# Kernel tuning notes

Measured on AMD Instinct MI355X. Metric: run time of the kernel, lower is better.

The kernel has to match this reference:

```python
import jax, jax.numpy as jnp
import numpy as np

B, N, F = 256, 64, 64
S = 2 * N + 2  # seq_len = N*2 + 2 = 130
EPS = 1e-6
SCALE = float(np.sqrt(S))


def _norm(x, alpha, beta):
    # custom Norm: mean/std over last axis, affine params shaped (F, S)
    m = jnp.mean(x, axis=-1, keepdims=True)
    s = jnp.std(x, axis=-1, keepdims=True)
    return alpha * (x - m) / (s + EPS) + beta


def setup_inputs() -> dict:
    key = jax.random.key(0)
    ks = jax.random.split(key, 12)
    d = {
        "sp": jax.random.normal(ks[0], (B, F), jnp.float32),
        "h1": jax.random.normal(ks[1], (B, N, F), jnp.float32),
        "h2": jax.random.normal(ks[2], (B, N, F), jnp.float32),
        # Dense(seq_len) kernels act on last axis of length S
        "Wq": jax.random.normal(ks[3], (S, S), jnp.float32) * 0.05,
        "bq": jnp.zeros((S,), jnp.float32),
        "Wk": jax.random.normal(ks[4], (S, S), jnp.float32) * 0.05,
        "bk": jnp.zeros((S,), jnp.float32),
        "Wv": jax.random.normal(ks[5], (S, S), jnp.float32) * 0.05,
        "bv": jnp.zeros((S,), jnp.float32),
        "alpha1": jnp.ones((F, S), jnp.float32),
        "beta1": jnp.zeros((F, S), jnp.float32),
        "alpha2": jnp.ones((F, S), jnp.float32),
        "beta2": jnp.zeros((F, S), jnp.float32),
        "Wlin": jax.random.normal(ks[6], (F * S, 1), jnp.float32) * 0.02,
        "blin": jnp.zeros((1,), jnp.float32),
    }
    return d


def reference(sp, h1, h2, Wq, bq, Wk, bk, Wv, bv,
              alpha1, beta1, alpha2, beta2, Wlin, blin):
    # obs: (B, 2N+1, F) -> transpose -> (B, F, 2N+1)
    obs = jnp.concatenate((h1, h2, sp[:, None, :]), axis=1).transpose(0, 2, 1)
    h2t = h2.transpose(0, 2, 1)  # (B, F, N): each action is a (B, F) column

    def fwd_action(action):  # action: (B, F)
        x = jnp.concatenate((obs, action[:, :, None]), axis=-1)  # (B, F, S)
        xn = _norm(x, alpha1, beta1)
        q = xn @ Wq + bq  # (B, F, S)
        k = xn @ Wk + bk
        v = xn @ Wv + bv
        # attention over the FEATURE axis: scores (B, F, F)
        sim = jnp.einsum('bis,bjs->bij', q, k) / SCALE
        p = jax.nn.softmax(sim, axis=-1)
        ao = jnp.einsum('bij,bjs->bis', p, v)  # (B, F, S)
        # deterministic dropout => residual is ao + ao
        y = _norm(ao + ao, alpha2, beta2)
        return y.reshape(B, -1) @ Wlin + blin  # (B, 1)

    q_values = jax.vmap(fwd_action, in_axes=-1, out_axes=1)(h2t)  # (B, N, 1)
    return q_values.reshape(B, N)
```

## Files before the change

kernel.cpp:

```cpp
#include <hip/hip_runtime.h>
#include <math.h>


typedef __attribute__((ext_vector_type(4))) float f32x4;
typedef __attribute__((ext_vector_type(8))) _Float16 h8;

#define EPSF 1e-6f
#define INVS 0.0877058019307029f

__device__ __forceinline__ unsigned short f2h(float f) {
  _Float16 h = (_Float16)f;
  return __builtin_bit_cast(unsigned short, h);
}
__device__ __forceinline__ float h2f(unsigned short s) {
  return (float)__builtin_bit_cast(_Float16, s);
}
__device__ __forceinline__ unsigned int pkh(float a, float b) {
  unsigned int r;
  asm("v_cvt_pkrtz_f16_f32 %0, %1, %2" : "=v"(r) : "v"(a), "v"(b));
  return r;
}

__global__ __launch_bounds__(256) void k0(
    const float* __restrict__ alpha1, const float* __restrict__ beta1,
    const float* __restrict__ alpha2, const float* __restrict__ beta2,
    const float* __restrict__ Wq, const float* __restrict__ bq,
    const float* __restrict__ Wk, const float* __restrict__ bk,
    const float* __restrict__ Wv, const float* __restrict__ bv,
    const float* __restrict__ Wlin, const float* __restrict__ blin,
    unsigned short* __restrict__ ABqk, unsigned short* __restrict__ ABv,
    unsigned short* __restrict__ AWt, float* __restrict__ Paw, float* __restrict__ Ccw)
{
  __shared__ float sbuf[64 * 132];
  __shared__ float Wbuf[130 * 144];
  int blk = blockIdx.x, tid = threadIdx.x;
  if (blk < 6) {
    int m = blk >> 1, isB = blk & 1;
    const float* src  = isB ? beta1 : alpha1;
    const float* W    = (m == 0) ? Wq : (m == 1) ? Wk : Wv;
    const float* bias = (m == 0) ? bq : (m == 1) ? bk : bv;
    for (int e = tid; e < 8320; e += 256) { int f = e / 130, s = e - f * 130; sbuf[f * 132 + s] = src[e]; }
    for (int e = tid; e < 16900; e += 256) { int s = e / 130, t = e - s * 130; Wbuf[s * 144 + t] = W[e]; }
    __syncthreads();
    int ty = tid >> 4, tx = tid & 15;
    float acc[4][9] = {};
    for (int s = 0; s < 130; ++s) {
      float g0 = sbuf[(ty * 4 + 0) * 132 + s];
      float g1 = sbuf[(ty * 4 + 1) * 132 + s];
      float g2 = sbuf[(ty * 4 + 2) * 132 + s];
      float g3 = sbuf[(ty * 4 + 3) * 132 + s];
#pragma unroll
      for (int c = 0; c < 9; ++c) {
        float wv = Wbuf[s * 144 + tx + 16 * c];
        acc[0][c] += g0 * wv; acc[1][c] += g1 * wv;
        acc[2][c] += g2 * wv; acc[3][c] += g3 * wv;
      }
    }
#pragma unroll
    for (int i = 0; i < 4; ++i)
      for (int c = 0; c < 9; ++c) {
        int t = tx + 16 * c;
        if (t < 136) {
          float val = (t < 130) ? (acc[i][c] + (isB ? bias[t] : 0.f)) : 0.f;
          unsigned short v16 = f2h(val);
          int f = ty * 4 + i;
          if (m == 2) ABv[t * 128 + isB * 64 + f] = v16;
          else        ABqk[(m * 64 + f) * 272 + (t >> 3) * 16 + isB * 8 + (t & 7)] = v16;
        }
      }
  } else if (blk == 6) {
    if (tid < 64) {
      int f = tid;
      float pa = 0.f, cc = 0.f;
      for (int s = 0; s < 130; ++s) {
        float wl = Wlin[f * 130 + s];
        float aw = alpha2[f * 130 + s] * wl;
        AWt[s * 72 + f] = f2h(aw);
        pa += aw;
        cc += beta2[f * 130 + s] * wl;
      }
      for (int s = 130; s < 144; ++s) AWt[s * 72 + f] = 0;
      Paw[f] = pa;
#pragma unroll
      for (int msk = 1; msk <= 32; msk <<= 1) cc += __shfl_xor(cc, msk, 64);
      if (f == 0) Ccw[0] = cc + blin[0];
    }
  }
}

__global__ __launch_bounds__(256) void k1(
    const float* __restrict__ h1, const float* __restrict__ h2,
    const float* __restrict__ sp, const float* __restrict__ alpha1,
    const float* __restrict__ Wq, const float* __restrict__ Wk, const float* __restrict__ Wv,
    unsigned short* __restrict__ UqkB, unsigned short* __restrict__ UvB,
    float* __restrict__ S1g, float* __restrict__ S2g)
{
  __shared__ float gbuf[64 * 132];
  __shared__ float Wbuf[130 * 144];
  __shared__ float ps[2][256];
  int b = blockIdx.x, tid = threadIdx.x;
  float s1 = 0.f, s2 = 0.f;
  for (int idx = tid; idx < 8256; idx += 256) {
    int s = idx >> 6, f = idx & 63;
    float x = (s < 64)  ? h1[((size_t)(b * 64 + s)) * 64 + f]
            : (s < 128) ? h2[((size_t)(b * 64 + (s - 64))) * 64 + f]
                        : sp[b * 64 + f];
    gbuf[f * 132 + s] = alpha1[f * 130 + s] * x;
    s1 += x; s2 += x * x;
  }
  ps[0][tid] = s1; ps[1][tid] = s2;
  __syncthreads();
  if (tid < 64) {
    S1g[b * 64 + tid] = ps[0][tid] + ps[0][tid + 64] + ps[0][tid + 128] + ps[0][tid + 192];
    S2g[b * 64 + tid] = ps[1][tid] + ps[1][tid + 64] + ps[1][tid + 128] + ps[1][tid + 192];
  }
  int ty = tid >> 4, tx = tid & 15;
  for (int m = 0; m < 3; ++m) {
    const float* W = (m == 0) ? Wq : (m == 1) ? Wk : Wv;
    __syncthreads();
    for (int e = tid; e < 16900; e += 256) { int s = e / 130, t = e - s * 130; Wbuf[s * 144 + t] = W[e]; }
    __syncthreads();
    float acc[4][9] = {};
    for (int s = 0; s < 129; ++s) {
      float g0 = gbuf[(ty * 4 + 0) * 132 + s];
      float g1 = gbuf[(ty * 4 + 1) * 132 + s];
      float g2 = gbuf[(ty * 4 + 2) * 132 + s];
      float g3 = gbuf[(ty * 4 + 3) * 132 + s];
#pragma unroll
      for (int c = 0; c < 9; ++c) {
        float wv = Wbuf[s * 144 + tx + 16 * c];
        acc[0][c] += g0 * wv; acc[1][c] += g1 * wv;
        acc[2][c] += g2 * wv; acc[3][c] += g3 * wv;
      }
    }
#pragma unroll
    for (int i = 0; i < 4; ++i)
      for (int c = 0; c < 9; ++c) {
        int t = tx + 16 * c;
        if (t < 136) {
          unsigned short v16 = f2h((t < 130) ? acc[i][c] : 0.f);
          int f = ty * 4 + i;
          if (m == 2) UvB[((size_t)b * 136 + t) * 64 + f] = v16;
          else        UqkB[(((size_t)b * 2 + m) * 64 + f) * 136 + t] = v16;
        }
      }
  }
}

__global__ __launch_bounds__(512, 2) void k2(
    const float* __restrict__ h2, const float* __restrict__ alpha1,
    const unsigned short* __restrict__ UqkB, const unsigned short* __restrict__ UvB,
    const unsigned short* __restrict__ ABqk, const unsigned short* __restrict__ ABv,
    const unsigned short* __restrict__ AWt,
    const float* __restrict__ S1g, const float* __restrict__ S2g,
    const float* __restrict__ Paw, const float* __restrict__ Ccw,
    const float* __restrict__ Wq, const float* __restrict__ Wk, const float* __restrict__ Wv,
    float* __restrict__ out)
{
  __shared__ __align__(16) unsigned short qb[64 * 168];
  __shared__ __align__(16) unsigned short kb[64 * 168];
  __shared__ __align__(16) unsigned short vT[144 * 72];
  __shared__ __align__(16) unsigned short pb[64 * 72];
  __shared__ __align__(16) unsigned short w129h[3][136];
  __shared__ float S1l[64], S2l[64], ael[64];
  __shared__ __align__(16) unsigned short mrow[64], irow[64], crow[64];
  __shared__ float redbuf[4];

  int bh = blockIdx.x;
  int b = bh >> 1, n0 = (bh & 1) << 5;
  int tid = threadIdx.x;
  int w = tid >> 6, l = tid & 63, l15 = l & 15, l4 = l >> 4;

  if (tid < 136) {
    w129h[0][tid] = (tid < 130) ? f2h(Wq[129 * 130 + tid]) : (unsigned short)0;
    w129h[1][tid] = (tid < 130) ? f2h(Wk[129 * 130 + tid]) : (unsigned short)0;
    w129h[2][tid] = (tid < 130) ? f2h(Wv[129 * 130 + tid]) : (unsigned short)0;
  }
  if (tid >= 256 && tid < 320) {
    int ff = tid - 256;
    float s1v = S1g[b * 64 + ff];
    float s2v = S2g[b * 64 + ff];
    float aev = alpha1[ff * 130 + 129];
    S1l[ff] = s1v; S2l[ff] = s2v; ael[ff] = aev;
    float a  = h2[((size_t)(b * 64 + n0)) * 64 + ff];
    float m  = (s1v + a) * (1.f / 130.f);
    float e2 = (s2v + a * a) * (1.f / 130.f);
    float sd = sqrtf(fmaxf(e2 - m * m, 0.f));
    mrow[ff] = f2h(m);
    irow[ff] = f2h(1.f / (sd + EPSF));
    crow[ff] = f2h(ael[ff] * a);
  }
  for (int i = tid; i < 64 * 24; i += 512) {
    int ff = i / 24, t = 136 + (i - ff * 24);
    qb[ff * 168 + t] = 0; kb[ff * 168 + t] = 0;
  }
  for (int i = tid; i < 14 * 72; i += 512) vT[130 * 72 + i] = 0;

  float awr[9][4], pawr[4];
  if (w < 4) {
#pragma unroll
    for (int sf = 0; sf < 9; ++sf)
#pragma unroll
      for (int rr = 0; rr < 4; ++rr)
        awr[sf][rr] = h2f(AWt[(sf * 16 + l15) * 72 + w * 16 + l4 * 4 + rr]);
#pragma unroll
    for (int rr = 0; rr < 4; ++rr) pawr[rr] = Paw[w * 16 + l4 * 4 + rr];
  }
  float ccv = Ccw[0];

  int isK = tid >> 8, t5 = tid & 255;
  const unsigned short* uqkg = UqkB + ((size_t)b * 2 + isK) * 64 * 136;
  const unsigned short* abg  = ABqk + isK * 64 * 272;
  const unsigned short* uvg  = UvB + (size_t)b * 136 * 64;
  unsigned short* dstqk = isK ? kb : qb;

  auto ldu = [&](int o) { int fo = o / 17, g = o - fo * 17;
                          return *(const h8*)(uqkg + fo * 136 + g * 8); };
  auto lda = [&](int o) { int fo = o / 17, g = o - fo * 17;
                          return *(const h8*)(abg + fo * 272 + g * 16); };
  auto ldb = [&](int o) { int fo = o / 17, g = o - fo * 17;
                          return *(const h8*)(abg + fo * 272 + g * 16 + 8); };
  h8 qU0 = ldu(t5),       qA0 = lda(t5),       qB0 = ldb(t5);
  h8 qU1 = ldu(t5 + 256), qA1 = lda(t5 + 256), qB1 = ldb(t5 + 256);
  h8 qU2 = ldu(t5 + 512), qA2 = lda(t5 + 512), qB2 = ldb(t5 + 512);
  h8 qU3 = ldu(t5 + 768), qA3 = lda(t5 + 768), qB3 = ldb(t5 + 768);
  h8 qUt = {}, qAt = {}, qBt = {};
  if (t5 < 64) { qUt = ldu(1024 + t5); qAt = lda(1024 + t5); qBt = ldb(1024 + t5); }
  auto ldvu = [&](int o) { int t = o >> 3, vf = o & 7;
                           return *(const h8*)(uvg + t * 64 + vf * 8); };
  auto ldva = [&](int o) { int t = o >> 3, vf = o & 7;
                           return *(const h8*)(ABv + t * 128 + (o & 7) * 8); };
  auto ldvb = [&](int o) { int t = o >> 3;
                           return *(const h8*)(ABv + t * 128 + 64 + (o & 7) * 8); };
  h8 vU0 = ldvu(tid),       vA0 = ldva(tid),       vB0 = ldvb(tid);
  h8 vU1 = ldvu(tid + 512), vA1 = ldva(tid + 512), vB1 = ldvb(tid + 512);
  h8 vUt = {}, vAt = {}, vBt = {};
  if (tid < 16) { vUt = ldvu(1024 + tid); vAt = ldva(1024 + tid); vBt = ldvb(1024 + tid); }

  __syncthreads();

  auto genqk = [&](int o, h8 uu, h8 aa, h8 bb) {
    int fo = o / 17, g = o - fo * 17;
    _Float16 m   = __builtin_bit_cast(_Float16, mrow[fo]);
    _Float16 inv = __builtin_bit_cast(_Float16, irow[fo]);
    _Float16 c   = __builtin_bit_cast(_Float16, crow[fo]);
    h8 ww = *(const h8*)(&w129h[isK][g * 8]);
    h8 res = (uu + c * ww - m * aa) * inv + bb;
    *(h8*)(dstqk + fo * 168 + g * 8) = res;
  };
  auto genv = [&](int o, h8 uu, h8 aa, h8 bb) {
    int t = o >> 3, vf = o & 7;
    _Float16 wv = __builtin_bit_cast(_Float16, w129h[2][t]);
    h8 mv = *(const h8*)(&mrow[vf * 8]);
    h8 iv = *(const h8*)(&irow[vf * 8]);
    h8 cv = *(const h8*)(&crow[vf * 8]);
    h8 res = (uu + cv * wv - mv * aa) * iv + bb;
    *(h8*)(&vT[t * 72 + vf * 8]) = res;
  };

  for (int n = n0; n < n0 + 32; ++n) {
    if (n > n0 && tid == 0)
      out[b * 64 + n - 1] = redbuf[0] + redbuf[1] + redbuf[2] + redbuf[3] + ccv;
    genqk(t5,       qU0, qA0, qB0);
    genqk(t5 + 256, qU1, qA1, qB1);
    genqk(t5 + 512, qU2, qA2, qB2);
    genqk(t5 + 768, qU3, qA3, qB3);
    if (t5 < 64) genqk(1024 + t5, qUt, qAt, qBt);
    genv(tid,       vU0, vA0, vB0);
    genv(tid + 512, vU1, vA1, vB1);
    if (tid < 16) genv(1024 + tid, vUt, vAt, vBt);
    __syncthreads();

    if (w < 4) {
      f32x4 sacc[4] = {};
      {
        const unsigned short* qrow = &qb[(w * 16 + l15) * 168 + l4 * 8];
#pragma unroll
        for (int kk = 0; kk < 5; ++kk) {
          h8 avv = *(const h8*)&qrow[kk * 32];
#pragma unroll
          for (int cf = 0; cf < 4; ++cf) {
            h8 bvv = *(const h8*)&kb[(cf * 16 + l15) * 168 + l4 * 8 + kk * 32];
            sacc[cf] = __builtin_amdgcn_mfma_f32_16x16x32_f16(avv, bvv, sacc[cf], 0, 0, 0);
          }
        }
      }
      float prob[4][4];
#pragma unroll
      for (int rr = 0; rr < 4; ++rr) {
        float ssum = 0.f;
#pragma unroll
        for (int cf = 0; cf < 4; ++cf) {
          float e = __expf(sacc[cf][rr] * INVS);
          prob[cf][rr] = e;
          ssum += e;
        }
#pragma unroll
        for (int msk = 1; msk <= 8; msk <<= 1) ssum += __shfl_xor(ssum, msk, 64);
        float is = 1.f / ssum;
#pragma unroll
        for (int cf = 0; cf < 4; ++cf) prob[cf][rr] *= is;
      }
#pragma unroll
      for (int cf = 0; cf < 4; ++cf) {
        unsigned int p01 = pkh(prob[cf][0], prob[cf][1]);
        unsigned int p23 = pkh(prob[cf][2], prob[cf][3]);
        int base = (w * 16 + l4 * 4) * 72 + cf * 16 + l15;
        pb[base]       = (unsigned short)p01;
        pb[base + 72]  = (unsigned short)(p01 >> 16);
        pb[base + 144] = (unsigned short)p23;
        pb[base + 216] = (unsigned short)(p23 >> 16);
      }

      f32x4 ao[9] = {};
      {
        const unsigned short* prow = &pb[(w * 16 + l15) * 72 + l4 * 8];
#pragma unroll
        for (int kk = 0; kk < 2; ++kk) {
          h8 avv = *(const h8*)&prow[kk * 32];
#pragma unroll
          for (int sf = 0; sf < 9; ++sf) {
            h8 bvv = *(const h8*)&vT[(sf * 16 + l15) * 72 + l4 * 8 + kk * 32];
            ao[sf] = __builtin_amdgcn_mfma_f32_16x16x32_f16(avv, bvv, ao[sf], 0, 0, 0);
          }
        }
      }
      float csum = 0.f;
#pragma unroll
      for (int rr = 0; rr < 4; ++rr) {
        float s1 = 0.f, s2 = 0.f, sdt = 0.f;
#pragma unroll
        for (int sf = 0; sf < 9; ++sf) {
          float v = ao[sf][rr];
          s1 += v; s2 += v * v; sdt += v * awr[sf][rr];
        }
#pragma unroll
        for (int msk = 1; msk <= 8; msk <<= 1) {
          s1 += __shfl_xor(s1, msk, 64);
          s2 += __shfl_xor(s2, msk, 64);
          sdt += __shfl_xor(sdt, msk, 64);
        }
        float mz  = 2.f * s1 * (1.f / 130.f);
        float ez2 = 4.f * s2 * (1.f / 130.f);
        float sg  = sqrtf(fmaxf(ez2 - mz * mz, 0.f));
        float i2  = 1.f / (sg + EPSF);
        csum += (2.f * sdt - mz * pawr[rr]) * i2;
      }
      csum += __shfl_xor(csum, 16, 64);
      csum += __shfl_xor(csum, 32, 64);
      if (l == 0) redbuf[w] = csum;
    } else if (w == 4 && n < n0 + 31) {
      int ff = l;
      float a  = h2[((size_t)(b * 64 + n + 1)) * 64 + ff];
      float m  = (S1l[ff] + a) * (1.f / 130.f);
      float e2 = (S2l[ff] + a * a) * (1.f / 130.f);
      float sd = sqrtf(fmaxf(e2 - m * m, 0.f));
      mrow[ff] = f2h(m);
      irow[ff] = f2h(1.f / (sd + EPSF));
      crow[ff] = f2h(ael[ff] * a);
    }
    __syncthreads();
  }
  if (tid == 0)
    out[b * 64 + n0 + 31] = redbuf[0] + redbuf[1] + redbuf[2] + redbuf[3] + ccv;
}

extern "C" void kernel_launch(void* const* d_in, const int* in_sizes, int n_in,
                              void* d_out, int out_size, void* d_ws, size_t ws_size,
                              hipStream_t stream) {
  const float* sp     = (const float*)d_in[0];
  const float* h1     = (const float*)d_in[1];
  const float* h2     = (const float*)d_in[2];
  const float* Wq     = (const float*)d_in[3];
  const float* bq     = (const float*)d_in[4];
  const float* Wk     = (const float*)d_in[5];
  const float* bk     = (const float*)d_in[6];
  const float* Wv     = (const float*)d_in[7];
  const float* bv     = (const float*)d_in[8];
  const float* alpha1 = (const float*)d_in[9];
  const float* beta1  = (const float*)d_in[10];
  const float* alpha2 = (const float*)d_in[11];
  const float* beta2  = (const float*)d_in[12];
  const float* Wlin   = (const float*)d_in[13];
  const float* blin   = (const float*)d_in[14];
  float* out = (float*)d_out;

  unsigned short* UqkB = (unsigned short*)d_ws;
  unsigned short* UvB  = UqkB + 4456448;
  unsigned short* ABqk = UvB + 2228224;
  unsigned short* ABv  = ABqk + 34816;
  unsigned short* AWt  = ABv + 17408;
  float* S1g = (float*)(AWt + 10368);
  float* S2g = S1g + 16384;
  float* Paw = S2g + 16384;
  float* Ccw = Paw + 64;

  k0<<<dim3(7), dim3(256), 0, stream>>>(alpha1, beta1, alpha2, beta2,
                                        Wq, bq, Wk, bk, Wv, bv, Wlin, blin,
                                        ABqk, ABv, AWt, Paw, Ccw);
  k1<<<dim3(256), dim3(256), 0, stream>>>(h1, h2, sp, alpha1, Wq, Wk, Wv,
                                          UqkB, UvB, S1g, S2g);
  k2<<<dim3(512), dim3(512), 0, stream>>>(h2, alpha1, UqkB, UvB, ABqk, ABv, AWt,
                                          S1g, S2g, Paw, Ccw,
                                          Wq, Wk, Wv, out);
}
```

Before: 343.5 us.

## Double-buffer q/k/v LDS tiles and process all actions per block

The q/k/v and norm-row shared buffers are double-buffered so each iteration generates the next action's tiles while computing the current one. This cuts the per-action loop from two barriers to one. Each block now handles all 64 actions of a batch row, so the grid shrinks from 512 to 256 blocks. The larger LDS footprint likely allows only one block per CU, which gives up the inter-block overlap the old two-blocks-per-CU layout provided and doubles the serial iterations per block.

```diff
diff --git a/kernel.cpp b/kernel.cpp
--- a/kernel.cpp
+++ b/kernel.cpp
@@ -157,18 +157,16 @@
     const float* __restrict__ Wq, const float* __restrict__ Wk, const float* __restrict__ Wv,
     float* __restrict__ out)
 {
-  __shared__ __align__(16) unsigned short qb[64 * 168];
-  __shared__ __align__(16) unsigned short kb[64 * 168];
-  __shared__ __align__(16) unsigned short vT[144 * 72];
+  __shared__ __align__(16) unsigned short qb[2][64 * 168];
+  __shared__ __align__(16) unsigned short kb[2][64 * 168];
+  __shared__ __align__(16) unsigned short vT[2][144 * 72];
   __shared__ __align__(16) unsigned short pb[64 * 72];
   __shared__ __align__(16) unsigned short w129h[3][136];
   __shared__ float S1l[64], S2l[64], ael[64];
-  __shared__ __align__(16) unsigned short mrow[64], irow[64], crow[64];
-  __shared__ float redbuf[4];
-
-  int bh = blockIdx.x;
-  int b = bh >> 1, n0 = (bh & 1) << 5;
-  int tid = threadIdx.x;
+  __shared__ __align__(16) unsigned short mrowB[2][64], irowB[2][64], crowB[2][64];
+  __shared__ float redbuf[2][4];
+
+  int b = blockIdx.x, tid = threadIdx.x;
   int w = tid >> 6, l = tid & 63, l15 = l & 15, l4 = l >> 4;
 
   if (tid < 136) {
@@ -176,25 +174,32 @@
     w129h[1][tid] = (tid < 130) ? f2h(Wk[129 * 130 + tid]) : (unsigned short)0;
     w129h[2][tid] = (tid < 130) ? f2h(Wv[129 * 130 + tid]) : (unsigned short)0;
   }
-  if (tid >= 256 && tid < 320) {
-    int ff = tid - 256;
-    float s1v = S1g[b * 64 + ff];
-    float s2v = S2g[b * 64 + ff];
-    float aev = alpha1[ff * 130 + 129];
-    S1l[ff] = s1v; S2l[ff] = s2v; ael[ff] = aev;
-    float a  = h2[((size_t)(b * 64 + n0)) * 64 + ff];
-    float m  = (s1v + a) * (1.f / 130.f);
-    float e2 = (s2v + a * a) * (1.f / 130.f);
+  if (tid >= 192 && tid < 256) {
+    int ff = tid - 192;
+    S1l[ff] = S1g[b * 64 + ff];
+    S2l[ff] = S2g[b * 64 + ff];
+    ael[ff] = alpha1[ff * 130 + 129];
+  }
+  if (tid < 128) {
+    int nn = tid >> 6, ff = tid & 63;
+    float a  = h2[((size_t)(b * 64 + nn)) * 64 + ff];
+    float s1 = S1g[b * 64 + ff], s2 = S2g[b * 64 + ff];
+    float m  = (s1 + a) * (1.f / 130.f);
+    float e2 = (s2 + a * a) * (1.f / 130.f);
     float sd = sqrtf(fmaxf(e2 - m * m, 0.f));
-    mrow[ff] = f2h(m);
-    irow[ff] = f2h(1.f / (sd + EPSF));
-    crow[ff] = f2h(ael[ff] * a);
-  }
-  for (int i = tid; i < 64 * 24; i += 512) {
-    int ff = i / 24, t = 136 + (i - ff * 24);
-    qb[ff * 168 + t] = 0; kb[ff * 168 + t] = 0;
-  }
-  for (int i = tid; i < 14 * 72; i += 512) vT[130 * 72 + i] = 0;
+    mrowB[nn][ff] = f2h(m);
+    irowB[nn][ff] = f2h(1.f / (sd + EPSF));
+    crowB[nn][ff] = f2h(alpha1[ff * 130 + 129] * a);
+  }
+  for (int i = tid; i < 2 * 64 * 24; i += 512) {
+    int c = i / (64 * 24), j = i - c * (64 * 24);
+    int ff = j / 24, t = 136 + (j - ff * 24);
+    qb[c][ff * 168 + t] = 0; kb[c][ff * 168 + t] = 0;
+  }
+  for (int i = tid; i < 2 * 14 * 72; i += 512) {
+    int c = i / (14 * 72), j = i - c * (14 * 72);
+    vT[c][130 * 72 + j] = 0;
+  }
 
   float awr[9][4], pawr[4];
   if (w < 4) {
@@ -212,7 +217,6 @@
   const unsigned short* uqkg = UqkB + ((size_t)b * 2 + isK) * 64 * 136;
   const unsigned short* abg  = ABqk + isK * 64 * 272;
   const unsigned short* uvg  = UvB + (size_t)b * 136 * 64;
-  unsigned short* dstqk = isK ? kb : qb;
 
   auto ldu = [&](int o) { int fo = o / 17, g = o - fo * 17;
                           return *(const h8*)(uqkg + fo * 136 + g * 8); };
@@ -229,9 +233,9 @@
   auto ldvu = [&](int o) { int t = o >> 3, vf = o & 7;
                            return *(const h8*)(uvg + t * 64 + vf * 8); };
   auto ldva = [&](int o) { int t = o >> 3, vf = o & 7;
-                           return *(const h8*)(ABv + t * 128 + (o & 7) * 8); };
-  auto ldvb = [&](int o) { int t = o >> 3;
-                           return *(const h8*)(ABv + t * 128 + 64 + (o & 7) * 8); };
+                           return *(const h8*)(ABv + t * 128 + vf * 8); };
+  auto ldvb = [&](int o) { int t = o >> 3, vf = o & 7;
+                           return *(const h8*)(ABv + t * 128 + 64 + vf * 8); };
   h8 vU0 = ldvu(tid),       vA0 = ldva(tid),       vB0 = ldvb(tid);
   h8 vU1 = ldvu(tid + 512), vA1 = ldva(tid + 512), vB1 = ldvb(tid + 512);
   h8 vUt = {}, vAt = {}, vBt = {};
@@ -239,48 +243,59 @@
 
   __syncthreads();
 
-  auto genqk = [&](int o, h8 uu, h8 aa, h8 bb) {
+  auto genqk = [&](int o, h8 uu, h8 aa, h8 bb, int sl, unsigned short* dstb) {
     int fo = o / 17, g = o - fo * 17;
-    _Float16 m   = __builtin_bit_cast(_Float16, mrow[fo]);
-    _Float16 inv = __builtin_bit_cast(_Float16, irow[fo]);
-    _Float16 c   = __builtin_bit_cast(_Float16, crow[fo]);
+    _Float16 m   = __builtin_bit_cast(_Float16, mrowB[sl][fo]);
+    _Float16 inv = __builtin_bit_cast(_Float16, irowB[sl][fo]);
+    _Float16 c   = __builtin_bit_cast(_Float16, crowB[sl][fo]);
     h8 ww = *(const h8*)(&w129h[isK][g * 8]);
     h8 res = (uu + c * ww - m * aa) * inv + bb;
-    *(h8*)(dstqk + fo * 168 + g * 8) = res;
+    *(h8*)(dstb + fo * 168 + g * 8) = res;
   };
-  auto genv = [&](int o, h8 uu, h8 aa, h8 bb) {
+  auto genv = [&](int o, h8 uu, h8 aa, h8 bb, int sl, unsigned short* vbase) {
     int t = o >> 3, vf = o & 7;
     _Float16 wv = __builtin_bit_cast(_Float16, w129h[2][t]);
-    h8 mv = *(const h8*)(&mrow[vf * 8]);
-    h8 iv = *(const h8*)(&irow[vf * 8]);
-    h8 cv = *(const h8*)(&crow[vf * 8]);
+    h8 mv = *(const h8*)(&mrowB[sl][vf * 8]);
+    h8 iv = *(const h8*)(&irowB[sl][vf * 8]);
+    h8 cv = *(const h8*)(&crowB[sl][vf * 8]);
     h8 res = (uu + cv * wv - mv * aa) * iv + bb;
-    *(h8*)(&vT[t * 72 + vf * 8]) = res;
+    *(h8*)(vbase + t * 72 + vf * 8) = res;
   };
-
-  for (int n = n0; n < n0 + 32; ++n) {
-    if (n > n0 && tid == 0)
-      out[b * 64 + n - 1] = redbuf[0] + redbuf[1] + redbuf[2] + redbuf[3] + ccv;
-    genqk(t5,       qU0, qA0, qB0);
-    genqk(t5 + 256, qU1, qA1, qB1);
-    genqk(t5 + 512, qU2, qA2, qB2);
-    genqk(t5 + 768, qU3, qA3, qB3);
-    if (t5 < 64) genqk(1024 + t5, qUt, qAt, qBt);
-    genv(tid,       vU0, vA0, vB0);
-    genv(tid + 512, vU1, vA1, vB1);
-    if (tid < 16) genv(1024 + tid, vUt, vAt, vBt);
-    __syncthreads();
+  auto regen_all = [&](int bufi, int sl) {
+    unsigned short* dq = isK ? kb[bufi] : qb[bufi];
+    genqk(t5,       qU0, qA0, qB0, sl, dq);
+    genqk(t5 + 256, qU1, qA1, qB1, sl, dq);
+    genqk(t5 + 512, qU2, qA2, qB2, sl, dq);
+    genqk(t5 + 768, qU3, qA3, qB3, sl, dq);
+    if (t5 < 64) genqk(1024 + t5, qUt, qAt, qBt, sl, dq);
+    genv(tid,       vU0, vA0, vB0, sl, vT[bufi]);
+    genv(tid + 512, vU1, vA1, vB1, sl, vT[bufi]);
+    if (tid < 16) genv(1024 + tid, vUt, vAt, vBt, sl, vT[bufi]);
+  };
+
+  regen_all(0, 0);
+  __syncthreads();
+
+  for (int n = 0; n < 64; ++n) {
+    int p = n & 1;
+    if (n > 0 && tid == 0)
+      out[b * 64 + n - 1] = redbuf[1 - p][0] + redbuf[1 - p][1]
+                          + redbuf[1 - p][2] + redbuf[1 - p][3] + ccv;
+    if (n < 63) regen_all(1 - p, 1 - p);
 
     if (w < 4) {
+      const unsigned short* qbp = qb[p];
+      const unsigned short* kbp = kb[p];
+      const unsigned short* vtp = vT[p];
       f32x4 sacc[4] = {};
       {
-        const unsigned short* qrow = &qb[(w * 16 + l15) * 168 + l4 * 8];
+        const unsigned short* qrow = &qbp[(w * 16 + l15) * 168 + l4 * 8];
 #pragma unroll
         for (int kk = 0; kk < 5; ++kk) {
           h8 avv = *(const h8*)&qrow[kk * 32];
 #pragma unroll
           for (int cf = 0; cf < 4; ++cf) {
-            h8 bvv = *(const h8*)&kb[(cf * 16 + l15) * 168 + l4 * 8 + kk * 32];
+            h8 bvv = *(const h8*)&kbp[(cf * 16 + l15) * 168 + l4 * 8 + kk * 32];
             sacc[cf] = __builtin_amdgcn_mfma_f32_16x16x32_f16(avv, bvv, sacc[cf], 0, 0, 0);
           }
         }
@@ -320,7 +335,7 @@
           h8 avv = *(const h8*)&prow[kk * 32];
 #pragma unroll
           for (int sf = 0; sf < 9; ++sf) {
-            h8 bvv = *(const h8*)&vT[(sf * 16 + l15) * 72 + l4 * 8 + kk * 32];
+            h8 bvv = *(const h8*)&vtp[(sf * 16 + l15) * 72 + l4 * 8 + kk * 32];
             ao[sf] = __builtin_amdgcn_mfma_f32_16x16x32_f16(avv, bvv, ao[sf], 0, 0, 0);
           }
         }
@@ -348,21 +363,21 @@
       }
       csum += __shfl_xor(csum, 16, 64);
       csum += __shfl_xor(csum, 32, 64);
-      if (l == 0) redbuf[w] = csum;
-    } else if (w == 4 && n < n0 + 31) {
+      if (l == 0) redbuf[p][w] = csum;
+    } else if (w == 4 && n < 62) {
       int ff = l;
-      float a  = h2[((size_t)(b * 64 + n + 1)) * 64 + ff];
+      float a  = h2[((size_t)(b * 64 + n + 2)) * 64 + ff];
       float m  = (S1l[ff] + a) * (1.f / 130.f);
       float e2 = (S2l[ff] + a * a) * (1.f / 130.f);
       float sd = sqrtf(fmaxf(e2 - m * m, 0.f));
-      mrow[ff] = f2h(m);
-      irow[ff] = f2h(1.f / (sd + EPSF));
-      crow[ff] = f2h(ael[ff] * a);
+      mrowB[p][ff] = f2h(m);
+      irowB[p][ff] = f2h(1.f / (sd + EPSF));
+      crowB[p][ff] = f2h(ael[ff] * a);
     }
     __syncthreads();
   }
   if (tid == 0)
-    out[b * 64 + n0 + 31] = redbuf[0] + redbuf[1] + redbuf[2] + redbuf[3] + ccv;
+    out[b * 64 + 63] = redbuf[1][0] + redbuf[1][1] + redbuf[1][2] + redbuf[1][3] + ccv;
 }
 
 extern "C" void kernel_launch(void* const* d_in, const int* in_sizes, int n_in,
@@ -400,7 +415,7 @@
                                         ABqk, ABv, AWt, Paw, Ccw);
   k1<<<dim3(256), dim3(256), 0, stream>>>(h1, h2, sp, alpha1, Wq, Wk, Wv,
                                           UqkB, UvB, S1g, S2g);
-  k2<<<dim3(512), dim3(512), 0, stream>>>(h2, alpha1, UqkB, UvB, ABqk, ABv, AWt,
+  k2<<<dim3(256), dim3(512), 0, stream>>>(h2, alpha1, UqkB, UvB, ABqk, ABv, AWt,
                                           S1g, S2g, Paw, Ccw,
                                           Wq, Wk, Wv, out);
 }
```

Result: faster. 316.5 us (-7.9%).
